# Performance work log

Measured on AMD Instinct MI355X. Metric: run time of the kernel, lower is better.

Reference implementation:

```python
import jax, jax.numpy as jnp
import numpy as np

N = 100000      # number of entities
E = 400000      # number of edges (before self-loops)
D = 200         # feature_dim
D0 = 100        # init_fea_dim
NREL = 475      # 2*num_rels + 1 (self-loop relation = NREL-1)
NBR = 100       # num_base_r
B = 1024        # query batch
L = 2           # number of cells / layers
EPS = 1e-5


def _bn(x, g, b):
    # BatchNorm1d, training-mode batch statistics (biased var), per-feature affine
    m = jnp.mean(x, axis=0)
    v = jnp.var(x, axis=0)
    return (x - m) * jax.lax.rsqrt(v + EPS) * g + b


def setup_inputs() -> dict:
    key = jax.random.key(0)
    ks = jax.random.split(key, 12)
    return {
        # graph (edge list form of the DGL graph g)
        "src_id": jax.random.randint(ks[0], (E,), 0, N),
        "dst_id": jax.random.randint(ks[1], (E,), 0, N),
        "e_type": jax.random.randint(ks[2], (E,), 0, NREL - 1),  # NREL-1 reserved for self-loop
        # link-prediction queries
        "subj": jax.random.randint(ks[3], (B,), 0, N),
        "rel": jax.random.randint(ks[4], (B,), 0, NREL),
        # learned parameters
        "emb_h": jax.random.normal(ks[5], (N, D0), dtype=jnp.float32) * 0.02,
        "emb_e": jax.random.normal(ks[6], (NBR, D), dtype=jnp.float32) * 0.1,
        "lin_w": jax.random.normal(ks[7], (D0, D), dtype=jnp.float32) * (1.0 / np.sqrt(D0)),
        "lin_b": jnp.zeros((D,), dtype=jnp.float32),
        "rel_wt": jax.random.normal(ks[8], (NREL, NBR), dtype=jnp.float32) * 0.1,
        "w_rel": jax.random.normal(ks[9], (D, D), dtype=jnp.float32) * (1.0 / np.sqrt(D)),
        # per-cell params, stacked over L layers
        "agg_bn_g": jnp.ones((L, D), dtype=jnp.float32),
        "agg_bn_b": jnp.zeros((L, D), dtype=jnp.float32),
        "cell_bn_g": jnp.ones((L, D), dtype=jnp.float32),
        "cell_bn_b": jnp.zeros((L, D), dtype=jnp.float32),
        "concat_w": jax.random.normal(ks[10], (L, D, D), dtype=jnp.float32) * (1.0 / np.sqrt(D)),
        "concat_b": jnp.zeros((L, D), dtype=jnp.float32),
    }


def reference(src_id, dst_id, e_type, subj, rel,
              emb_h, emb_e, lin_w, lin_b, rel_wt, w_rel,
              agg_bn_g, agg_bn_b, cell_bn_g, cell_bn_b, concat_w, concat_b):
    nodes = jnp.arange(N, dtype=src_id.dtype)
    # append self-loops for every node, with the dedicated self-loop relation id
    src_f = jnp.concatenate([src_id, nodes])                      # [E+N]
    dst_f = jnp.concatenate([dst_id, nodes])                      # [E+N]
    et_f = jnp.concatenate([e_type, jnp.full((N,), NREL - 1, dtype=e_type.dtype)])

    all_ent = emb_h @ lin_w + lin_b                               # [N, D]
    rel_embed = rel_wt @ emb_e                                    # [NREL, D]

    for i in range(L):
        src_emb = all_ent[src_f]                                  # [E+N, D] per-edge gather
        hr = rel_embed[et_f]                                      # [E+N, D] per-edge gather
        zero_out = src_emb * hr                                   # pre_mult op (no BN/ReLU)
        agg = jax.ops.segment_sum(zero_out, dst_f, num_segments=N)  # edge -> node aggregation
        agg = jax.nn.relu(_bn(agg, agg_bn_g[i], agg_bn_b[i]))     # OpModule BN + ReLU
        h = agg @ concat_w[i] + concat_b[i]                       # Cell concat Linear (1 concat node)
        all_ent = jax.nn.relu(_bn(h, cell_bn_g[i], cell_bn_b[i]))  # Cell BN + ReLU
        rel_embed = rel_embed @ w_rel                             # per-layer relation transform

    # DistMult score function: [B, N]
    score = (all_ent[subj] * rel_embed[rel]) @ all_ent.T
    return score
```

## Files before the change

kernel.cpp:

```cpp
#include <hip/hip_runtime.h>


#define N_ENT  100000
#define N_EDGE 400000
#define N_EF   500000
#define D_     200
#define D0_    100
#define NREL_  475
#define B_     1024
#define GSTAT  1024
#define KP_D   224
#define KP_D0  128

typedef unsigned short ushort_t;
typedef __attribute__((ext_vector_type(8))) short bf16x8;
typedef __attribute__((ext_vector_type(4))) float f32x4;

__device__ __forceinline__ ushort_t f2bf(float x) {
  unsigned u = __float_as_uint(x);
  return (ushort_t)((u + 0x7FFFu + ((u >> 16) & 1u)) >> 16);
}
__device__ __forceinline__ float bf2f(ushort_t h) {
  return __uint_as_float(((unsigned)h) << 16);
}

__device__ __forceinline__ void gld16(const void* g, void* l) {
  __builtin_amdgcn_global_load_lds(
      (const __attribute__((address_space(1))) unsigned*)g,
      (__attribute__((address_space(3))) unsigned*)l, 16, 0, 0);
}


__global__ void k_hist(const int* __restrict__ dst_id, int* __restrict__ cnt) {
  int e = blockIdx.x * 256 + threadIdx.x;
  if (e < N_EF) {
    int d = (e < N_EDGE) ? dst_id[e] : (e - N_EDGE);
    atomicAdd(&cnt[d], 1);
  }
}

__global__ __launch_bounds__(256) void k_scan_block(const int* __restrict__ cnt,
                                                    int* __restrict__ rp,
                                                    int* __restrict__ bsum) {
  __shared__ int sm[256];
  int tid = threadIdx.x;
  int base = blockIdx.x * 1024 + tid * 4;
  int v0 = (base + 0 < N_ENT) ? cnt[base + 0] : 0;
  int v1 = (base + 1 < N_ENT) ? cnt[base + 1] : 0;
  int v2 = (base + 2 < N_ENT) ? cnt[base + 2] : 0;
  int v3 = (base + 3 < N_ENT) ? cnt[base + 3] : 0;
  int tsum = v0 + v1 + v2 + v3;
  sm[tid] = tsum;
  __syncthreads();
  for (int off = 1; off < 256; off <<= 1) {
    int t = (tid >= off) ? sm[tid - off] : 0;
    __syncthreads();
    sm[tid] += t;
    __syncthreads();
  }
  int run = sm[tid] - tsum;
  if (base + 0 < N_ENT) { rp[base + 0] = run; } run += v0;
  if (base + 1 < N_ENT) { rp[base + 1] = run; } run += v1;
  if (base + 2 < N_ENT) { rp[base + 2] = run; } run += v2;
  if (base + 3 < N_ENT) { rp[base + 3] = run; }
  if (tid == 255) bsum[blockIdx.x] = sm[255];
}

__global__ void k_scan_tops(int* __restrict__ bsum, int nb) {
  __shared__ int sm[256];
  int tid = threadIdx.x;
  int v = (tid < nb) ? bsum[tid] : 0;
  sm[tid] = v;
  __syncthreads();
  for (int off = 1; off < 256; off <<= 1) {
    int t = (tid >= off) ? sm[tid - off] : 0;
    __syncthreads();
    sm[tid] += t;
    __syncthreads();
  }
  if (tid < nb) bsum[tid] = sm[tid] - v;
}

__global__ void k_scan_add(int* __restrict__ rp, const int* __restrict__ bsum,
                           int* __restrict__ cursor) {
  int i = blockIdx.x * 256 + threadIdx.x;
  if (i < N_ENT) {
    int r = rp[i] + bsum[i >> 10];
    rp[i] = r;
    cursor[i] = r;
  }
}

__global__ void k_fill(const int* __restrict__ src_id, const int* __restrict__ dst_id,
                       const int* __restrict__ e_type, int* __restrict__ cursor,
                       int* __restrict__ cs, int* __restrict__ ct) {
  int e = blockIdx.x * 256 + threadIdx.x;
  if (e < N_EF) {
    int s, d, t;
    if (e < N_EDGE) { s = src_id[e]; d = dst_id[e]; t = e_type[e]; }
    else            { s = e - N_EDGE; d = s; t = NREL_ - 1; }
    int pos = atomicAdd(&cursor[d], 1);
    cs[pos] = s;
    ct[pos] = t;
  }
}


__global__ __launch_bounds__(256) void k_aggregate(const float* __restrict__ ent,
                                                   const float* __restrict__ relE,
                                                   const int* __restrict__ rp,
                                                   const int* __restrict__ cnt,
                                                   const int* __restrict__ cs,
                                                   const int* __restrict__ ct,
                                                   float* __restrict__ out) {
  int n = blockIdx.x;
  int f = threadIdx.x;
  if (f >= D_) return;
  int s0 = rp[n], e0 = s0 + cnt[n];
  float acc0 = 0.f, acc1 = 0.f;
  int idx = s0;
  for (; idx + 2 <= e0; idx += 2) {
    int sA = cs[idx], tA = ct[idx];
    int sB = cs[idx + 1], tB = ct[idx + 1];
    float eA = ent[(long)sA * D_ + f], rA = relE[(long)tA * D_ + f];
    float eB = ent[(long)sB * D_ + f], rB = relE[(long)tB * D_ + f];
    acc0 = fmaf(eA, rA, acc0);
    acc1 = fmaf(eB, rB, acc1);
  }
  if (idx < e0) {
    int sA = cs[idx], tA = ct[idx];
    acc0 = fmaf(ent[(long)sA * D_ + f], relE[(long)tA * D_ + f], acc0);
  }
  out[(long)n * D_ + f] = acc0 + acc1;
}

__global__ __launch_bounds__(256) void k_colstats(const float* __restrict__ X,
                                                  double* __restrict__ part) {
  int f = threadIdx.x;
  if (f >= D_) return;
  double s = 0.0, s2 = 0.0;
  for (int r = blockIdx.x; r < N_ENT; r += GSTAT) {
    float v = X[(long)r * D_ + f];
    s += v;
    s2 += (double)v * v;
  }
  part[(long)blockIdx.x * (2 * D_) + f] = s;
  part[(long)blockIdx.x * (2 * D_) + D_ + f] = s2;
}

__global__ __launch_bounds__(256) void k_bn_fin(const double* __restrict__ part,
                                                const float* __restrict__ g,
                                                const float* __restrict__ b,
                                                float* __restrict__ scale,
                                                float* __restrict__ shift) {
  int f = blockIdx.x;
  int tid = threadIdx.x;
  double S = 0.0, S2 = 0.0;
  for (int i = tid; i < GSTAT; i += 256) {
    S += part[(long)i * (2 * D_) + f];
    S2 += part[(long)i * (2 * D_) + D_ + f];
  }
  __shared__ double smS[256], smS2[256];
  smS[tid] = S; smS2[tid] = S2;
  __syncthreads();
  for (int off = 128; off > 0; off >>= 1) {
    if (tid < off) { smS[tid] += smS[tid + off]; smS2[tid] += smS2[tid + off]; }
    __syncthreads();
  }
  if (tid == 0) {
    double mean = smS[0] / N_ENT;
    double var = smS2[0] / N_ENT - mean * mean;
    double inv = 1.0 / sqrt(var + 1e-5);
    float sc = g[f] * (float)inv;
    scale[f] = sc;
    shift[f] = b[f] - (float)mean * sc;
  }
}

template <bool SPLIT>
__global__ void k_norm_relu(float* __restrict__ X, const float* __restrict__ scale,
                            const float* __restrict__ shift,
                            ushort_t* __restrict__ H, ushort_t* __restrict__ L) {
  if (!SPLIT) {
    const long total = (long)N_ENT * D_ / 4;
    for (long i4 = (long)blockIdx.x * 256 + threadIdx.x; i4 < total;
         i4 += (long)gridDim.x * 256) {
      float4 v = ((float4*)X)[i4];
      int fb = (int)((i4 * 4) % D_);
      v.x = fmaxf(fmaf(v.x, scale[fb + 0], shift[fb + 0]), 0.f);
      v.y = fmaxf(fmaf(v.y, scale[fb + 1], shift[fb + 1]), 0.f);
      v.z = fmaxf(fmaf(v.z, scale[fb + 2], shift[fb + 2]), 0.f);
      v.w = fmaxf(fmaf(v.w, scale[fb + 3], shift[fb + 3]), 0.f);
      ((float4*)X)[i4] = v;
    }
  } else {
    const long total = (long)N_ENT * (KP_D / 4);
    for (long i4 = (long)blockIdx.x * 256 + threadIdx.x; i4 < total;
         i4 += (long)gridDim.x * 256) {
      int r = (int)(i4 / (KP_D / 4));
      int c4 = (int)(i4 % (KP_D / 4)) * 4;
      float vv[4] = {0.f, 0.f, 0.f, 0.f};
      if (c4 < D_) {
        float4 v = *(float4*)(X + (long)r * D_ + c4);
        vv[0] = fmaxf(fmaf(v.x, scale[c4 + 0], shift[c4 + 0]), 0.f);
        vv[1] = fmaxf(fmaf(v.y, scale[c4 + 1], shift[c4 + 1]), 0.f);
        vv[2] = fmaxf(fmaf(v.z, scale[c4 + 2], shift[c4 + 2]), 0.f);
        vv[3] = fmaxf(fmaf(v.w, scale[c4 + 3], shift[c4 + 3]), 0.f);
        float4 o = make_float4(vv[0], vv[1], vv[2], vv[3]);
        *(float4*)(X + (long)r * D_ + c4) = o;
      }
      unsigned hpack0, hpack1, lpack0, lpack1;
      ushort_t h[4], l[4];
#pragma unroll
      for (int t = 0; t < 4; t++) {
        h[t] = f2bf(vv[t]);
        l[t] = f2bf(vv[t] - bf2f(h[t]));
      }
      hpack0 = (unsigned)h[0] | ((unsigned)h[1] << 16);
      hpack1 = (unsigned)h[2] | ((unsigned)h[3] << 16);
      lpack0 = (unsigned)l[0] | ((unsigned)l[1] << 16);
      lpack1 = (unsigned)l[2] | ((unsigned)l[3] << 16);
      long o = (long)r * KP_D + c4;
      *(uint2*)(H + o) = make_uint2(hpack0, hpack1);
      *(uint2*)(L + o) = make_uint2(lpack0, lpack1);
    }
  }
}


__global__ void k_split(const float* __restrict__ X, int R, int K, int Kp,
                        ushort_t* __restrict__ H, ushort_t* __restrict__ L,
                        const float* __restrict__ scale,
                        const float* __restrict__ shift) {
  int kq = Kp >> 2;
  long i = (long)blockIdx.x * 256 + threadIdx.x;
  if (i >= (long)R * kq) return;
  int r = (int)(i / kq);
  int k4 = (int)(i % kq) * 4;
  float vv[4] = {0.f, 0.f, 0.f, 0.f};
  if (k4 < K) {
    float4 v = *(const float4*)(X + (long)r * K + k4);
    vv[0] = v.x; vv[1] = v.y; vv[2] = v.z; vv[3] = v.w;
    if (scale) {
#pragma unroll
      for (int t = 0; t < 4; t++)
        vv[t] = fmaxf(fmaf(vv[t], scale[k4 + t], shift[k4 + t]), 0.f);
    }
  }
  ushort_t h[4], l[4];
#pragma unroll
  for (int t = 0; t < 4; t++) {
    h[t] = f2bf(vv[t]);
    l[t] = f2bf(vv[t] - bf2f(h[t]));
  }
  long o = (long)r * Kp + k4;
  *(uint2*)(H + o) = make_uint2((unsigned)h[0] | ((unsigned)h[1] << 16),
                                (unsigned)h[2] | ((unsigned)h[3] << 16));
  *(uint2*)(L + o) = make_uint2((unsigned)l[0] | ((unsigned)l[1] << 16),
                                (unsigned)l[2] | ((unsigned)l[3] << 16));
}

__global__ void k_tsplit(const float* __restrict__ W, int K, int Nc, int Kp,
                         ushort_t* __restrict__ H, ushort_t* __restrict__ L) {
  int i = blockIdx.x * 256 + threadIdx.x;
  if (i >= Nc * Kp) return;
  int n = i / Kp, kp = i - n * Kp;
  float v = (kp < K) ? W[(long)kp * Nc + n] : 0.f;
  ushort_t h = f2bf(v);
  H[i] = h;
  L[i] = f2bf(v - bf2f(h));
}

__global__ void k_qsplit(const float* __restrict__ ent, const float* __restrict__ relE,
                         const int* __restrict__ subj, const int* __restrict__ rel,
                         ushort_t* __restrict__ H, ushort_t* __restrict__ L) {
  int i = blockIdx.x * 256 + threadIdx.x;
  if (i >= B_ * KP_D) return;
  int b = i / KP_D, kp = i - b * KP_D;
  float v = 0.f;
  if (kp < D_)
    v = ent[(long)subj[b] * D_ + kp] * relE[(long)rel[b] * D_ + kp];
  ushort_t h = f2bf(v);
  H[i] = h;
  L[i] = f2bf(v - bf2f(h));
}

template <bool HAS_BIAS, bool SWZ>
__global__ __launch_bounds__(256, 2) void k_mfma_abt(
    const ushort_t* __restrict__ Ah, const ushort_t* __restrict__ Al,
    const ushort_t* __restrict__ Bh, const ushort_t* __restrict__ Bl,
    float* __restrict__ C, int M, int Nc, int Kp, long ldc,
    const float* __restrict__ bias) {
  __shared__ ushort_t lds[4 * 128 * 32];
  const int tid = threadIdx.x;
  const int wave = tid >> 6, lane = tid & 63;
  int bxi, byi;
  if (SWZ) {
    int orig = blockIdx.x;
    int cpx = gridDim.x >> 3;
    int swz = (orig & 7) * cpx + (orig >> 3);
    bxi = swz & 7;
    byi = swz >> 3;
  } else {
    bxi = blockIdx.x;
    byi = blockIdx.y;
  }
  const int bm = bxi * 128, bn = byi * 128;
  const int wr = (wave >> 1) * 64, wc = (wave & 1) * 64;
  const int l15 = lane & 15, l4 = lane >> 4;

  f32x4 acc[4][4] = {};

  for (int kc = 0; kc < Kp; kc += 32) {
#pragma unroll
    for (int j = 0; j < 8; ++j) {
      int c = wave * 8 + j;
      int buf = c >> 3;
      int r = (c & 7) * 16 + (lane >> 2);
      int sg = (lane & 3) ^ ((r >> 1) & 3);
      const ushort_t* bp;
      int rowg;
      if (buf == 0)      { bp = Ah; rowg = bm + r; if (rowg > M - 1) rowg = M - 1; }
      else if (buf == 1) { bp = Al; rowg = bm + r; if (rowg > M - 1) rowg = M - 1; }
      else if (buf == 2) { bp = Bh; rowg = bn + r; if (rowg > Nc - 1) rowg = Nc - 1; }
      else               { bp = Bl; rowg = bn + r; if (rowg > Nc - 1) rowg = Nc - 1; }
      const ushort_t* g = bp + (long)rowg * Kp + kc + sg * 8;
      gld16(g, lds + c * 512);
    }
    __syncthreads();

    bf16x8 a_h[4], a_l[4], b_h[4], b_l[4];
#pragma unroll
    for (int i = 0; i < 4; i++) {
      int rA = wr + i * 16 + l15;
      int sA = (l4 ^ ((rA >> 1) & 3)) * 8;
      a_h[i] = *(const bf16x8*)(lds + rA * 32 + sA);
      a_l[i] = *(const bf16x8*)(lds + 4096 + rA * 32 + sA);
      int rB = wc + i * 16 + l15;
      int sB = (l4 ^ ((rB >> 1) & 3)) * 8;
      b_h[i] = *(const bf16x8*)(lds + 8192 + rB * 32 + sB);
      b_l[i] = *(const bf16x8*)(lds + 12288 + rB * 32 + sB);
    }
#pragma unroll
    for (int i = 0; i < 4; i++)
#pragma unroll
      for (int j = 0; j < 4; j++) {
        acc[i][j] = __builtin_amdgcn_mfma_f32_16x16x32_bf16(a_h[i], b_h[j], acc[i][j], 0, 0, 0);
        acc[i][j] = __builtin_amdgcn_mfma_f32_16x16x32_bf16(a_l[i], b_h[j], acc[i][j], 0, 0, 0);
        acc[i][j] = __builtin_amdgcn_mfma_f32_16x16x32_bf16(a_h[i], b_l[j], acc[i][j], 0, 0, 0);
      }
    __syncthreads();
  }

#pragma unroll
  for (int i = 0; i < 4; i++) {
    int mrow = bm + wr + i * 16 + l4 * 4;
#pragma unroll
    for (int j = 0; j < 4; j++) {
      int n = bn + wc + j * 16 + l15;
      if (n >= Nc) continue;
      float bb = HAS_BIAS ? bias[n] : 0.f;
#pragma unroll
      for (int v = 0; v < 4; v++) {
        int m = mrow + v;
        if (m < M) C[(long)m * ldc + n] = acc[i][j][v] + bb;
      }
    }
  }
}

template <int TM, int TN>
__global__ __launch_bounds__(256) void k_gemm_abt(
    const float* __restrict__ A, const float* __restrict__ Bm, float* __restrict__ C,
    int M, int Nc, int K, long ldc) {
  constexpr int BM = TM * 16, BN = TN * 16, KC = 20;
  __shared__ float As[BM * KC];
  __shared__ float Bs[BN * KC];
  const int tid = threadIdx.x;
  const int tx = tid & 15, ty = tid >> 4;
  const int bm = blockIdx.x * BM, bn = blockIdx.y * BN;
  float acc[TM][TN];
#pragma unroll
  for (int i = 0; i < TM; i++)
#pragma unroll
    for (int j = 0; j < TN; j++) acc[i][j] = 0.f;
  for (int kc = 0; kc < K; kc += KC) {
    for (int i4 = tid; i4 < BM * 5; i4 += 256) {
      int r = i4 / 5, kq = (i4 - r * 5) * 4;
      int row = bm + r; if (row > M - 1) row = M - 1;
      *(float4*)(As + r * KC + kq) = *(const float4*)(A + (long)row * K + kc + kq);
    }
    for (int i4 = tid; i4 < BN * 5; i4 += 256) {
      int r = i4 / 5, kq = (i4 - r * 5) * 4;
      int row = bn + r; if (row > Nc - 1) row = Nc - 1;
      *(float4*)(Bs + r * KC + kq) = *(const float4*)(Bm + (long)row * K + kc + kq);
    }
    __syncthreads();
#pragma unroll
    for (int k4 = 0; k4 < KC; k4 += 4) {
      float4 af[TM], bf[TN];
#pragma unroll
      for (int i = 0; i < TM; i++) af[i] = *(const float4*)(As + (i * 16 + ty) * KC + k4);
#pragma unroll
      for (int j = 0; j < TN; j++) bf[j] = *(const float4*)(Bs + (j * 16 + tx) * KC + k4);
#pragma unroll
      for (int i = 0; i < TM; i++)
#pragma unroll
        for (int j = 0; j < TN; j++) {
          acc[i][j] = fmaf(af[i].x, bf[j].x, acc[i][j]);
          acc[i][j] = fmaf(af[i].y, bf[j].y, acc[i][j]);
          acc[i][j] = fmaf(af[i].z, bf[j].z, acc[i][j]);
          acc[i][j] = fmaf(af[i].w, bf[j].w, acc[i][j]);
        }
    }
    __syncthreads();
  }
#pragma unroll
  for (int i = 0; i < TM; i++) {
    int m = bm + i * 16 + ty;
    if (m >= M) continue;
#pragma unroll
    for (int j = 0; j < TN; j++) {
      int n = bn + j * 16 + tx;
      if (n < Nc) C[(long)m * ldc + n] = acc[i][j];
    }
  }
}

__global__ void k_transpose(const float* __restrict__ s, float* __restrict__ d, int R, int C) {
  int i = blockIdx.x * 256 + threadIdx.x;
  if (i < R * C) { int r = i / C, c = i - r * C; d[c * R + r] = s[i]; }
}


extern "C" void kernel_launch(void* const* d_in, const int* in_sizes, int n_in,
                              void* d_out, int out_size, void* d_ws, size_t ws_size,
                              hipStream_t stream) {
  const int* src_id = (const int*)d_in[0];
  const int* dst_id = (const int*)d_in[1];
  const int* e_type = (const int*)d_in[2];
  const int* subj = (const int*)d_in[3];
  const int* rel = (const int*)d_in[4];
  const float* emb_h = (const float*)d_in[5];
  const float* emb_e = (const float*)d_in[6];
  const float* lin_w = (const float*)d_in[7];
  const float* lin_b = (const float*)d_in[8];
  const float* rel_wt = (const float*)d_in[9];
  const float* w_rel = (const float*)d_in[10];
  const float* agg_bn_g = (const float*)d_in[11];
  const float* agg_bn_b = (const float*)d_in[12];
  const float* cell_bn_g = (const float*)d_in[13];
  const float* cell_bn_b = (const float*)d_in[14];
  const float* concat_w = (const float*)d_in[15];
  const float* concat_b = (const float*)d_in[16];
  float* out = (float*)d_out;

  char* w = (char*)d_ws;
  ushort_t* ent_h = (ushort_t*)(w + 0);
  ushort_t* ent_l = (ushort_t*)(w + 44800000);
  ushort_t* q_h   = (ushort_t*)(w + 89600000);
  ushort_t* q_l   = (ushort_t*)(w + 90112000);

  char* ob = (char*)d_out;
  float* ent    = (float*)(ob + 0);
  float* tmp    = (float*)(ob + 80000000);
  ushort_t* tmp_h = (ushort_t*)(ob + 160000000);
  ushort_t* tmp_l = (ushort_t*)(ob + 204800000);
  ushort_t* embh_h = (ushort_t*)(ob + 160000000);
  ushort_t* embh_l = (ushort_t*)(ob + 185600000);
  int* counts  = (int*)(ob + 249600000);
  int* row_ptr = (int*)(ob + 250000000);
  int* cursor  = (int*)(ob + 250400000);
  int* csr_src = (int*)(ob + 250800000);
  int* csr_et  = (int*)(ob + 252800000);
  double* part = (double*)(ob + 254800000);
  float* relA  = (float*)(ob + 258100000);
  float* relB  = (float*)(ob + 258480000);
  float* embeT = (float*)(ob + 258860000);
  float* wrT   = (float*)(ob + 258940000);
  ushort_t* linw_h = (ushort_t*)(ob + 259100000);
  ushort_t* linw_l = (ushort_t*)(ob + 259151200);
  ushort_t* cw0_h  = (ushort_t*)(ob + 259202400);
  ushort_t* cw0_l  = (ushort_t*)(ob + 259292000);
  ushort_t* cw1_h  = (ushort_t*)(ob + 259381600);
  ushort_t* cw1_l  = (ushort_t*)(ob + 259471200);
  float* scaleb = (float*)(ob + 259560800);
  float* shiftb = (float*)(ob + 259561696);
  int* bsum     = (int*)(ob + 259562592);

  hipMemsetAsync(counts, 0, N_ENT * sizeof(int), stream);
  k_hist<<<(N_EF + 255) / 256, 256, 0, stream>>>(dst_id, counts);
  const int NB = (N_ENT + 1023) / 1024;
  k_scan_block<<<NB, 256, 0, stream>>>(counts, row_ptr, bsum);
  k_scan_tops<<<1, 256, 0, stream>>>(bsum, NB);
  k_scan_add<<<(N_ENT + 255) / 256, 256, 0, stream>>>(row_ptr, bsum, cursor);
  k_fill<<<(N_EF + 255) / 256, 256, 0, stream>>>(src_id, dst_id, e_type, cursor,
                                                 csr_src, csr_et);

  k_tsplit<<<(D_ * KP_D0 + 255) / 256, 256, 0, stream>>>(lin_w, D0_, D_, KP_D0,
                                                         linw_h, linw_l);
  k_tsplit<<<(D_ * KP_D + 255) / 256, 256, 0, stream>>>(concat_w, D_, D_, KP_D,
                                                        cw0_h, cw0_l);
  k_tsplit<<<(D_ * KP_D + 255) / 256, 256, 0, stream>>>(concat_w + D_ * D_, D_, D_,
                                                        KP_D, cw1_h, cw1_l);
  k_transpose<<<(D0_ * D_ + 255) / 256, 256, 0, stream>>>(emb_e, embeT, D0_, D_);
  k_transpose<<<(D_ * D_ + 255) / 256, 256, 0, stream>>>(w_rel, wrT, D_, D_);

  const int GM = (N_ENT + 127) / 128;
  {
    long tot = (long)N_ENT * (KP_D0 / 4);
    k_split<<<(int)((tot + 255) / 256), 256, 0, stream>>>(emb_h, N_ENT, D0_, KP_D0,
                                                          embh_h, embh_l, nullptr, nullptr);
    k_mfma_abt<true, false><<<dim3(GM, 2), 256, 0, stream>>>(
        embh_h, embh_l, linw_h, linw_l, ent, N_ENT, D_, KP_D0, (long)D_, lin_b);
  }
  k_gemm_abt<8, 4><<<dim3(4, 4), 256, 0, stream>>>(rel_wt, embeT, relA, NREL_, D_,
                                                   D0_, (long)D_);

  float* relCur = relA;
  float* relNxt = relB;
  for (int i = 0; i < 2; i++) {
    k_aggregate<<<N_ENT, 256, 0, stream>>>(ent, relCur, row_ptr, counts, csr_src,
                                           csr_et, tmp);
    k_colstats<<<GSTAT, 256, 0, stream>>>(tmp, part);
    k_bn_fin<<<D_, 256, 0, stream>>>(part, agg_bn_g + i * D_, agg_bn_b + i * D_,
                                     scaleb, shiftb);
    long tot = (long)N_ENT * (KP_D / 4);
    k_split<<<(int)((tot + 255) / 256), 256, 0, stream>>>(tmp, N_ENT, D_, KP_D,
                                                          tmp_h, tmp_l, scaleb, shiftb);
    k_mfma_abt<true, false><<<dim3(GM, 2), 256, 0, stream>>>(
        tmp_h, tmp_l, (i == 0) ? cw0_h : cw1_h, (i == 0) ? cw0_l : cw1_l, ent,
        N_ENT, D_, KP_D, (long)D_, concat_b + i * D_);
    k_colstats<<<GSTAT, 256, 0, stream>>>(ent, part);
    k_bn_fin<<<D_, 256, 0, stream>>>(part, cell_bn_g + i * D_, cell_bn_b + i * D_,
                                     scaleb, shiftb);
    if (i == 0) {
      k_norm_relu<false><<<2048, 256, 0, stream>>>(ent, scaleb, shiftb, nullptr, nullptr);
    } else {
      k_norm_relu<true><<<2048, 256, 0, stream>>>(ent, scaleb, shiftb, ent_h, ent_l);
    }
    k_gemm_abt<8, 4><<<dim3(4, 4), 256, 0, stream>>>(relCur, wrT, relNxt, NREL_, D_,
                                                     D_, (long)D_);
    float* t = relCur; relCur = relNxt; relNxt = t;
  }

  k_qsplit<<<(B_ * KP_D + 255) / 256, 256, 0, stream>>>(ent, relCur, subj, rel,
                                                        q_h, q_l);

  k_mfma_abt<false, true><<<dim3((B_ / 128) * GM), 256, 0, stream>>>(
      q_h, q_l, ent_h, ent_l, out, B_, N_ENT, KP_D, (long)N_ENT, nullptr);
}
```

Before: 1.123 ms.

## Fuse BN+split into GEMM A-load, double-buffer MFMA, fold layer-0 BN into aggregate

The per-layer GEMMs now read fp32 activations directly, apply the BN scale/shift and ReLU, and split to bf16 hi/lo in registers while staging into LDS. This removes the separate k_split passes and their bf16 buffers. The layer-0 cell BN+ReLU is folded into the layer-1 gather, so the standalone normalize pass is dropped. The MFMA kernels gain LDS double buffering to overlap loads with compute, the aggregate loop is unrolled to 4 edges, and colstats uses float4 rows with more blocks. In exchange, the BN transform is recomputed per gathered edge, and the GEMMs use more LDS and registers.

```diff
diff --git a/kernel.cpp b/kernel.cpp
--- a/kernel.cpp
+++ b/kernel.cpp
@@ -8,7 +8,7 @@
 #define D0_    100
 #define NREL_  475
 #define B_     1024
-#define GSTAT  1024
+#define GSTAT2 2048
 #define KP_D   224
 #define KP_D0  128
 
@@ -106,46 +106,68 @@
 }
 
 
+template <bool BN>
 __global__ __launch_bounds__(256) void k_aggregate(const float* __restrict__ ent,
                                                    const float* __restrict__ relE,
                                                    const int* __restrict__ rp,
                                                    const int* __restrict__ cnt,
                                                    const int* __restrict__ cs,
                                                    const int* __restrict__ ct,
-                                                   float* __restrict__ out) {
+                                                   float* __restrict__ out,
+                                                   const float* __restrict__ scale,
+                                                   const float* __restrict__ shift) {
   int n = blockIdx.x;
   int f = threadIdx.x;
   if (f >= D_) return;
+  float sc = 0.f, sh = 0.f;
+  if (BN) { sc = scale[f]; sh = shift[f]; }
   int s0 = rp[n], e0 = s0 + cnt[n];
-  float acc0 = 0.f, acc1 = 0.f;
+  float a0 = 0.f, a1 = 0.f, a2 = 0.f, a3 = 0.f;
   int idx = s0;
-  for (; idx + 2 <= e0; idx += 2) {
-    int sA = cs[idx], tA = ct[idx];
+  for (; idx + 4 <= e0; idx += 4) {
+    int sA = cs[idx + 0], tA = ct[idx + 0];
     int sB = cs[idx + 1], tB = ct[idx + 1];
+    int sC = cs[idx + 2], tC = ct[idx + 2];
+    int sD = cs[idx + 3], tD = ct[idx + 3];
     float eA = ent[(long)sA * D_ + f], rA = relE[(long)tA * D_ + f];
     float eB = ent[(long)sB * D_ + f], rB = relE[(long)tB * D_ + f];
-    acc0 = fmaf(eA, rA, acc0);
-    acc1 = fmaf(eB, rB, acc1);
-  }
-  if (idx < e0) {
+    float eC = ent[(long)sC * D_ + f], rC = relE[(long)tC * D_ + f];
+    float eD = ent[(long)sD * D_ + f], rD = relE[(long)tD * D_ + f];
+    if (BN) {
+      eA = fmaxf(fmaf(eA, sc, sh), 0.f);
+      eB = fmaxf(fmaf(eB, sc, sh), 0.f);
+      eC = fmaxf(fmaf(eC, sc, sh), 0.f);
+      eD = fmaxf(fmaf(eD, sc, sh), 0.f);
+    }
+    a0 = fmaf(eA, rA, a0);
+    a1 = fmaf(eB, rB, a1);
+    a2 = fmaf(eC, rC, a2);
+    a3 = fmaf(eD, rD, a3);
+  }
+  for (; idx < e0; ++idx) {
     int sA = cs[idx], tA = ct[idx];
-    acc0 = fmaf(ent[(long)sA * D_ + f], relE[(long)tA * D_ + f], acc0);
-  }
-  out[(long)n * D_ + f] = acc0 + acc1;
-}
-
-__global__ __launch_bounds__(256) void k_colstats(const float* __restrict__ X,
-                                                  double* __restrict__ part) {
-  int f = threadIdx.x;
-  if (f >= D_) return;
-  double s = 0.0, s2 = 0.0;
-  for (int r = blockIdx.x; r < N_ENT; r += GSTAT) {
-    float v = X[(long)r * D_ + f];
-    s += v;
-    s2 += (double)v * v;
-  }
-  part[(long)blockIdx.x * (2 * D_) + f] = s;
-  part[(long)blockIdx.x * (2 * D_) + D_ + f] = s2;
+    float eA = ent[(long)sA * D_ + f];
+    if (BN) eA = fmaxf(fmaf(eA, sc, sh), 0.f);
+    a0 = fmaf(eA, relE[(long)tA * D_ + f], a0);
+  }
+  out[(long)n * D_ + f] = (a0 + a1) + (a2 + a3);
+}
+
+__global__ __launch_bounds__(64) void k_colstats(const float* __restrict__ X,
+                                                 double* __restrict__ part) {
+  int t = threadIdx.x;
+  if (t >= 50) return;
+  double s0 = 0, s1 = 0, s2 = 0, s3 = 0, q0 = 0, q1 = 0, q2 = 0, q3 = 0;
+  for (int r = blockIdx.x; r < N_ENT; r += GSTAT2) {
+    float4 v = *(const float4*)(X + (long)r * D_ + t * 4);
+    s0 += v.x; q0 += (double)v.x * v.x;
+    s1 += v.y; q1 += (double)v.y * v.y;
+    s2 += v.z; q2 += (double)v.z * v.z;
+    s3 += v.w; q3 += (double)v.w * v.w;
+  }
+  long o = (long)blockIdx.x * 400 + t * 4;
+  part[o + 0] = s0; part[o + 1] = s1; part[o + 2] = s2; part[o + 3] = s3;
+  part[o + 200] = q0; part[o + 201] = q1; part[o + 202] = q2; part[o + 203] = q3;
 }
 
 __global__ __launch_bounds__(256) void k_bn_fin(const double* __restrict__ part,
@@ -156,9 +178,9 @@
   int f = blockIdx.x;
   int tid = threadIdx.x;
   double S = 0.0, S2 = 0.0;
-  for (int i = tid; i < GSTAT; i += 256) {
-    S += part[(long)i * (2 * D_) + f];
-    S2 += part[(long)i * (2 * D_) + D_ + f];
+  for (int i = tid; i < GSTAT2; i += 256) {
+    S += part[(long)i * 400 + f];
+    S2 += part[(long)i * 400 + 200 + f];
   }
   __shared__ double smS[256], smS2[256];
   smS[tid] = S; smS2[tid] = S2;
@@ -177,87 +199,35 @@
   }
 }
 
-template <bool SPLIT>
-__global__ void k_norm_relu(float* __restrict__ X, const float* __restrict__ scale,
-                            const float* __restrict__ shift,
-                            ushort_t* __restrict__ H, ushort_t* __restrict__ L) {
-  if (!SPLIT) {
-    const long total = (long)N_ENT * D_ / 4;
-    for (long i4 = (long)blockIdx.x * 256 + threadIdx.x; i4 < total;
-         i4 += (long)gridDim.x * 256) {
-      float4 v = ((float4*)X)[i4];
-      int fb = (int)((i4 * 4) % D_);
-      v.x = fmaxf(fmaf(v.x, scale[fb + 0], shift[fb + 0]), 0.f);
-      v.y = fmaxf(fmaf(v.y, scale[fb + 1], shift[fb + 1]), 0.f);
-      v.z = fmaxf(fmaf(v.z, scale[fb + 2], shift[fb + 2]), 0.f);
-      v.w = fmaxf(fmaf(v.w, scale[fb + 3], shift[fb + 3]), 0.f);
-      ((float4*)X)[i4] = v;
-    }
-  } else {
-    const long total = (long)N_ENT * (KP_D / 4);
-    for (long i4 = (long)blockIdx.x * 256 + threadIdx.x; i4 < total;
-         i4 += (long)gridDim.x * 256) {
-      int r = (int)(i4 / (KP_D / 4));
-      int c4 = (int)(i4 % (KP_D / 4)) * 4;
-      float vv[4] = {0.f, 0.f, 0.f, 0.f};
-      if (c4 < D_) {
-        float4 v = *(float4*)(X + (long)r * D_ + c4);
-        vv[0] = fmaxf(fmaf(v.x, scale[c4 + 0], shift[c4 + 0]), 0.f);
-        vv[1] = fmaxf(fmaf(v.y, scale[c4 + 1], shift[c4 + 1]), 0.f);
-        vv[2] = fmaxf(fmaf(v.z, scale[c4 + 2], shift[c4 + 2]), 0.f);
-        vv[3] = fmaxf(fmaf(v.w, scale[c4 + 3], shift[c4 + 3]), 0.f);
-        float4 o = make_float4(vv[0], vv[1], vv[2], vv[3]);
-        *(float4*)(X + (long)r * D_ + c4) = o;
-      }
-      unsigned hpack0, hpack1, lpack0, lpack1;
-      ushort_t h[4], l[4];
-#pragma unroll
-      for (int t = 0; t < 4; t++) {
-        h[t] = f2bf(vv[t]);
-        l[t] = f2bf(vv[t] - bf2f(h[t]));
-      }
-      hpack0 = (unsigned)h[0] | ((unsigned)h[1] << 16);
-      hpack1 = (unsigned)h[2] | ((unsigned)h[3] << 16);
-      lpack0 = (unsigned)l[0] | ((unsigned)l[1] << 16);
-      lpack1 = (unsigned)l[2] | ((unsigned)l[3] << 16);
-      long o = (long)r * KP_D + c4;
-      *(uint2*)(H + o) = make_uint2(hpack0, hpack1);
-      *(uint2*)(L + o) = make_uint2(lpack0, lpack1);
-    }
-  }
-}
-
-
-__global__ void k_split(const float* __restrict__ X, int R, int K, int Kp,
-                        ushort_t* __restrict__ H, ushort_t* __restrict__ L,
-                        const float* __restrict__ scale,
-                        const float* __restrict__ shift) {
-  int kq = Kp >> 2;
-  long i = (long)blockIdx.x * 256 + threadIdx.x;
-  if (i >= (long)R * kq) return;
-  int r = (int)(i / kq);
-  int k4 = (int)(i % kq) * 4;
-  float vv[4] = {0.f, 0.f, 0.f, 0.f};
-  if (k4 < K) {
-    float4 v = *(const float4*)(X + (long)r * K + k4);
-    vv[0] = v.x; vv[1] = v.y; vv[2] = v.z; vv[3] = v.w;
-    if (scale) {
-#pragma unroll
-      for (int t = 0; t < 4; t++)
-        vv[t] = fmaxf(fmaf(vv[t], scale[k4 + t], shift[k4 + t]), 0.f);
-    }
-  }
-  ushort_t h[4], l[4];
-#pragma unroll
-  for (int t = 0; t < 4; t++) {
-    h[t] = f2bf(vv[t]);
-    l[t] = f2bf(vv[t] - bf2f(h[t]));
-  }
-  long o = (long)r * Kp + k4;
-  *(uint2*)(H + o) = make_uint2((unsigned)h[0] | ((unsigned)h[1] << 16),
-                                (unsigned)h[2] | ((unsigned)h[3] << 16));
-  *(uint2*)(L + o) = make_uint2((unsigned)l[0] | ((unsigned)l[1] << 16),
-                                (unsigned)l[2] | ((unsigned)l[3] << 16));
+__global__ void k_norm_split(float* __restrict__ X, const float* __restrict__ scale,
+                             const float* __restrict__ shift,
+                             ushort_t* __restrict__ H, ushort_t* __restrict__ L) {
+  const long total = (long)N_ENT * (KP_D / 4);
+  for (long i4 = (long)blockIdx.x * 256 + threadIdx.x; i4 < total;
+       i4 += (long)gridDim.x * 256) {
+    int r = (int)(i4 / (KP_D / 4));
+    int c4 = (int)(i4 % (KP_D / 4)) * 4;
+    float vv[4] = {0.f, 0.f, 0.f, 0.f};
+    if (c4 < D_) {
+      float4 v = *(float4*)(X + (long)r * D_ + c4);
+      vv[0] = fmaxf(fmaf(v.x, scale[c4 + 0], shift[c4 + 0]), 0.f);
+      vv[1] = fmaxf(fmaf(v.y, scale[c4 + 1], shift[c4 + 1]), 0.f);
+      vv[2] = fmaxf(fmaf(v.z, scale[c4 + 2], shift[c4 + 2]), 0.f);
+      vv[3] = fmaxf(fmaf(v.w, scale[c4 + 3], shift[c4 + 3]), 0.f);
+      *(float4*)(X + (long)r * D_ + c4) = make_float4(vv[0], vv[1], vv[2], vv[3]);
+    }
+    ushort_t h[4], l[4];
+#pragma unroll
+    for (int t = 0; t < 4; t++) {
+      h[t] = f2bf(vv[t]);
+      l[t] = f2bf(vv[t] - bf2f(h[t]));
+    }
+    long o = (long)r * KP_D + c4;
+    *(uint2*)(H + o) = make_uint2((unsigned)h[0] | ((unsigned)h[1] << 16),
+                                  (unsigned)h[2] | ((unsigned)h[3] << 16));
+    *(uint2*)(L + o) = make_uint2((unsigned)l[0] | ((unsigned)l[1] << 16),
+                                  (unsigned)l[2] | ((unsigned)l[3] << 16));
+  }
 }
 
 __global__ void k_tsplit(const float* __restrict__ W, int K, int Nc, int Kp,
@@ -285,13 +255,12 @@
   L[i] = f2bf(v - bf2f(h));
 }
 
-template <bool HAS_BIAS, bool SWZ>
-__global__ __launch_bounds__(256, 2) void k_mfma_abt(
+template <bool SWZ>
+__global__ __launch_bounds__(256, 2) void k_mfma_pre(
     const ushort_t* __restrict__ Ah, const ushort_t* __restrict__ Al,
     const ushort_t* __restrict__ Bh, const ushort_t* __restrict__ Bl,
-    float* __restrict__ C, int M, int Nc, int Kp, long ldc,
-    const float* __restrict__ bias) {
-  __shared__ ushort_t lds[4 * 128 * 32];
+    float* __restrict__ C, int M, int Nc, int Kp, long ldc) {
+  __shared__ __align__(16) ushort_t lds[2 * 16384];
   const int tid = threadIdx.x;
   const int wave = tid >> 6, lane = tid & 63;
   int bxi, byi;
@@ -308,10 +277,11 @@
   const int bm = bxi * 128, bn = byi * 128;
   const int wr = (wave >> 1) * 64, wc = (wave & 1) * 64;
   const int l15 = lane & 15, l4 = lane >> 4;
+  const int NT = Kp >> 5;
 
   f32x4 acc[4][4] = {};
 
-  for (int kc = 0; kc < Kp; kc += 32) {
+  auto stage = [&](int kt, int ph) {
 #pragma unroll
     for (int j = 0; j < 8; ++j) {
       int c = wave * 8 + j;
@@ -324,22 +294,27 @@
       else if (buf == 1) { bp = Al; rowg = bm + r; if (rowg > M - 1) rowg = M - 1; }
       else if (buf == 2) { bp = Bh; rowg = bn + r; if (rowg > Nc - 1) rowg = Nc - 1; }
       else               { bp = Bl; rowg = bn + r; if (rowg > Nc - 1) rowg = Nc - 1; }
-      const ushort_t* g = bp + (long)rowg * Kp + kc + sg * 8;
-      gld16(g, lds + c * 512);
-    }
-    __syncthreads();
-
+      gld16(bp + (long)rowg * Kp + kt * 32 + sg * 8, lds + ph * 16384 + c * 512);
+    }
+  };
+
+  stage(0, 0);
+  __syncthreads();
+  int p = 0;
+  for (int t = 0; t < NT; ++t) {
+    if (t + 1 < NT) stage(t + 1, p ^ 1);
+    const ushort_t* base = lds + p * 16384;
     bf16x8 a_h[4], a_l[4], b_h[4], b_l[4];
 #pragma unroll
     for (int i = 0; i < 4; i++) {
       int rA = wr + i * 16 + l15;
       int sA = (l4 ^ ((rA >> 1) & 3)) * 8;
-      a_h[i] = *(const bf16x8*)(lds + rA * 32 + sA);
-      a_l[i] = *(const bf16x8*)(lds + 4096 + rA * 32 + sA);
+      a_h[i] = *(const bf16x8*)(base + rA * 32 + sA);
+      a_l[i] = *(const bf16x8*)(base + 4096 + rA * 32 + sA);
       int rB = wc + i * 16 + l15;
       int sB = (l4 ^ ((rB >> 1) & 3)) * 8;
-      b_h[i] = *(const bf16x8*)(lds + 8192 + rB * 32 + sB);
-      b_l[i] = *(const bf16x8*)(lds + 12288 + rB * 32 + sB);
+      b_h[i] = *(const bf16x8*)(base + 8192 + rB * 32 + sB);
+      b_l[i] = *(const bf16x8*)(base + 12288 + rB * 32 + sB);
     }
 #pragma unroll
     for (int i = 0; i < 4; i++)
@@ -350,6 +325,158 @@
         acc[i][j] = __builtin_amdgcn_mfma_f32_16x16x32_bf16(a_h[i], b_l[j], acc[i][j], 0, 0, 0);
       }
     __syncthreads();
+    p ^= 1;
+  }
+
+#pragma unroll
+  for (int i = 0; i < 4; i++) {
+    int mrow = bm + wr + i * 16 + l4 * 4;
+#pragma unroll
+    for (int j = 0; j < 4; j++) {
+      int n = bn + wc + j * 16 + l15;
+      if (n >= Nc) continue;
+#pragma unroll
+      for (int v = 0; v < 4; v++) {
+        int m = mrow + v;
+        if (m < M) C[(long)m * ldc + n] = acc[i][j][v];
+      }
+    }
+  }
+}
+
+template <bool BN_A, bool HAS_BIAS>
+__global__ __launch_bounds__(256, 2) void k_mfma_af32(
+    const float* __restrict__ A, int lda, int K,
+    const ushort_t* __restrict__ Bh, const ushort_t* __restrict__ Bl,
+    float* __restrict__ C, int M, int Nc, int Kp, long ldc,
+    const float* __restrict__ scale, const float* __restrict__ shift,
+    const float* __restrict__ bias) {
+  __shared__ __align__(16) ushort_t lds[2 * 16384];
+  __shared__ float sc_lds[KP_D], sh_lds[KP_D];
+  const int tid = threadIdx.x;
+  const int wave = tid >> 6, lane = tid & 63;
+  const int bm = blockIdx.x * 128, bn = blockIdx.y * 128;
+  const int wr = (wave >> 1) * 64, wc = (wave & 1) * 64;
+  const int l15 = lane & 15, l4 = lane >> 4;
+  const int NT = Kp >> 5;
+
+  if (BN_A) {
+    for (int i = tid; i < Kp; i += 256) {
+      sc_lds[i] = (i < K) ? scale[i] : 0.f;
+      sh_lds[i] = (i < K) ? shift[i] : 0.f;
+    }
+    __syncthreads();
+  }
+
+  const int ar = tid >> 1;
+  const int acb = (tid & 1) * 16;
+  int arow = bm + ar; if (arow > M - 1) arow = M - 1;
+  const int aswz = (ar >> 1) & 3;
+  const int s0 = (((acb >> 3) + 0) ^ aswz) * 8;
+  const int s1 = (((acb >> 3) + 1) ^ aswz) * 8;
+
+  auto loadA = [&](int kt, float4* va) {
+    int kc = kt * 32 + acb;
+    const float* ap = A + (long)arow * lda + kc;
+    if (kc + 16 <= K) {
+#pragma unroll
+      for (int q = 0; q < 4; q++) va[q] = *(const float4*)(ap + q * 4);
+    } else {
+#pragma unroll
+      for (int q = 0; q < 4; q++) {
+        float t0 = (kc + q * 4 + 0 < K) ? ap[q * 4 + 0] : 0.f;
+        float t1 = (kc + q * 4 + 1 < K) ? ap[q * 4 + 1] : 0.f;
+        float t2 = (kc + q * 4 + 2 < K) ? ap[q * 4 + 2] : 0.f;
+        float t3 = (kc + q * 4 + 3 < K) ? ap[q * 4 + 3] : 0.f;
+        va[q] = make_float4(t0, t1, t2, t3);
+      }
+    }
+  };
+
+  auto writeA = [&](int kt, int ph, float4* va) {
+    float v[16];
+#pragma unroll
+    for (int q = 0; q < 4; q++) {
+      v[q * 4 + 0] = va[q].x; v[q * 4 + 1] = va[q].y;
+      v[q * 4 + 2] = va[q].z; v[q * 4 + 3] = va[q].w;
+    }
+    if (BN_A) {
+      int kc = kt * 32 + acb;
+#pragma unroll
+      for (int e = 0; e < 16; e++) {
+        int col = kc + e;
+        if (col < K) v[e] = fmaxf(fmaf(v[e], sc_lds[col], sh_lds[col]), 0.f);
+      }
+    }
+    unsigned hh[8], ll[8];
+#pragma unroll
+    for (int e = 0; e < 8; e++) {
+      ushort_t h0 = f2bf(v[2 * e]), h1 = f2bf(v[2 * e + 1]);
+      ushort_t l0 = f2bf(v[2 * e] - bf2f(h0)), l1 = f2bf(v[2 * e + 1] - bf2f(h1));
+      hh[e] = (unsigned)h0 | ((unsigned)h1 << 16);
+      ll[e] = (unsigned)l0 | ((unsigned)l1 << 16);
+    }
+    ushort_t* baseA = lds + ph * 16384 + ar * 32;
+    *(uint4*)(baseA + s0) = make_uint4(hh[0], hh[1], hh[2], hh[3]);
+    *(uint4*)(baseA + s1) = make_uint4(hh[4], hh[5], hh[6], hh[7]);
+    ushort_t* baseL = baseA + 4096;
+    *(uint4*)(baseL + s0) = make_uint4(ll[0], ll[1], ll[2], ll[3]);
+    *(uint4*)(baseL + s1) = make_uint4(ll[4], ll[5], ll[6], ll[7]);
+  };
+
+  auto stageB = [&](int kt, int ph) {
+#pragma unroll
+    for (int j = 0; j < 4; ++j) {
+      int c = 16 + wave * 4 + j;
+      int buf = c >> 3;
+      int r = (c & 7) * 16 + (lane >> 2);
+      int sg = (lane & 3) ^ ((r >> 1) & 3);
+      const ushort_t* bp = (buf == 2) ? Bh : Bl;
+      int rowg = bn + r; if (rowg > Nc - 1) rowg = Nc - 1;
+      gld16(bp + (long)rowg * Kp + kt * 32 + sg * 8, lds + ph * 16384 + c * 512);
+    }
+  };
+
+  f32x4 acc[4][4] = {};
+  {
+    float4 va[4];
+    loadA(0, va);
+    writeA(0, 0, va);
+    stageB(0, 0);
+  }
+  __syncthreads();
+  int p = 0;
+  for (int t = 0; t < NT; ++t) {
+    float4 va[4];
+    const bool pre = (t + 1 < NT);
+    if (pre) {
+      loadA(t + 1, va);
+      stageB(t + 1, p ^ 1);
+    }
+    const ushort_t* base = lds + p * 16384;
+    bf16x8 a_h[4], a_l[4], b_h[4], b_l[4];
+#pragma unroll
+    for (int i = 0; i < 4; i++) {
+      int rA = wr + i * 16 + l15;
+      int sA = (l4 ^ ((rA >> 1) & 3)) * 8;
+      a_h[i] = *(const bf16x8*)(base + rA * 32 + sA);
+      a_l[i] = *(const bf16x8*)(base + 4096 + rA * 32 + sA);
+      int rB = wc + i * 16 + l15;
+      int sB = (l4 ^ ((rB >> 1) & 3)) * 8;
+      b_h[i] = *(const bf16x8*)(base + 8192 + rB * 32 + sB);
+      b_l[i] = *(const bf16x8*)(base + 12288 + rB * 32 + sB);
+    }
+#pragma unroll
+    for (int i = 0; i < 4; i++)
+#pragma unroll
+      for (int j = 0; j < 4; j++) {
+        acc[i][j] = __builtin_amdgcn_mfma_f32_16x16x32_bf16(a_h[i], b_h[j], acc[i][j], 0, 0, 0);
+        acc[i][j] = __builtin_amdgcn_mfma_f32_16x16x32_bf16(a_l[i], b_h[j], acc[i][j], 0, 0, 0);
+        acc[i][j] = __builtin_amdgcn_mfma_f32_16x16x32_bf16(a_h[i], b_l[j], acc[i][j], 0, 0, 0);
+      }
+    if (pre) writeA(t + 1, p ^ 1, va);
+    __syncthreads();
+    p ^= 1;
   }
 
 #pragma unroll
@@ -464,29 +591,25 @@
   char* ob = (char*)d_out;
   float* ent    = (float*)(ob + 0);
   float* tmp    = (float*)(ob + 80000000);
-  ushort_t* tmp_h = (ushort_t*)(ob + 160000000);
-  ushort_t* tmp_l = (ushort_t*)(ob + 204800000);
-  ushort_t* embh_h = (ushort_t*)(ob + 160000000);
-  ushort_t* embh_l = (ushort_t*)(ob + 185600000);
-  int* counts  = (int*)(ob + 249600000);
-  int* row_ptr = (int*)(ob + 250000000);
-  int* cursor  = (int*)(ob + 250400000);
-  int* csr_src = (int*)(ob + 250800000);
-  int* csr_et  = (int*)(ob + 252800000);
-  double* part = (double*)(ob + 254800000);
-  float* relA  = (float*)(ob + 258100000);
-  float* relB  = (float*)(ob + 258480000);
-  float* embeT = (float*)(ob + 258860000);
-  float* wrT   = (float*)(ob + 258940000);
-  ushort_t* linw_h = (ushort_t*)(ob + 259100000);
-  ushort_t* linw_l = (ushort_t*)(ob + 259151200);
-  ushort_t* cw0_h  = (ushort_t*)(ob + 259202400);
-  ushort_t* cw0_l  = (ushort_t*)(ob + 259292000);
-  ushort_t* cw1_h  = (ushort_t*)(ob + 259381600);
-  ushort_t* cw1_l  = (ushort_t*)(ob + 259471200);
-  float* scaleb = (float*)(ob + 259560800);
-  float* shiftb = (float*)(ob + 259561696);
-  int* bsum     = (int*)(ob + 259562592);
+  double* part  = (double*)(ob + 160000000);
+  int* counts   = (int*)(ob + 166600000);
+  int* row_ptr  = (int*)(ob + 167000000);
+  int* cursor   = (int*)(ob + 167400000);
+  int* csr_src  = (int*)(ob + 167800000);
+  int* csr_et   = (int*)(ob + 169800000);
+  float* relA   = (float*)(ob + 171800000);
+  float* relB   = (float*)(ob + 172180000);
+  float* embeT  = (float*)(ob + 172560000);
+  float* wrT    = (float*)(ob + 172640000);
+  ushort_t* linw_h = (ushort_t*)(ob + 172800000);
+  ushort_t* linw_l = (ushort_t*)(ob + 172851200);
+  ushort_t* cw0_h  = (ushort_t*)(ob + 172902400);
+  ushort_t* cw0_l  = (ushort_t*)(ob + 172992000);
+  ushort_t* cw1_h  = (ushort_t*)(ob + 173081600);
+  ushort_t* cw1_l  = (ushort_t*)(ob + 173171200);
+  float* scaleb = (float*)(ob + 173260800);
+  float* shiftb = (float*)(ob + 173261824);
+  int* bsum     = (int*)(ob + 173262848);
 
   hipMemsetAsync(counts, 0, N_ENT * sizeof(int), stream);
   k_hist<<<(N_EF + 255) / 256, 256, 0, stream>>>(dst_id, counts);
@@ -507,46 +630,41 @@
   k_transpose<<<(D_ * D_ + 255) / 256, 256, 0, stream>>>(w_rel, wrT, D_, D_);
 
   const int GM = (N_ENT + 127) / 128;
-  {
-    long tot = (long)N_ENT * (KP_D0 / 4);
-    k_split<<<(int)((tot + 255) / 256), 256, 0, stream>>>(emb_h, N_ENT, D0_, KP_D0,
-                                                          embh_h, embh_l, nullptr, nullptr);
-    k_mfma_abt<true, false><<<dim3(GM, 2), 256, 0, stream>>>(
-        embh_h, embh_l, linw_h, linw_l, ent, N_ENT, D_, KP_D0, (long)D_, lin_b);
-  }
+
+  k_mfma_af32<false, true><<<dim3(GM, 2), 256, 0, stream>>>(
+      emb_h, D0_, D0_, linw_h, linw_l, ent, N_ENT, D_, KP_D0, (long)D_,
+      nullptr, nullptr, lin_b);
   k_gemm_abt<8, 4><<<dim3(4, 4), 256, 0, stream>>>(rel_wt, embeT, relA, NREL_, D_,
                                                    D0_, (long)D_);
 
-  float* relCur = relA;
-  float* relNxt = relB;
-  for (int i = 0; i < 2; i++) {
-    k_aggregate<<<N_ENT, 256, 0, stream>>>(ent, relCur, row_ptr, counts, csr_src,
-                                           csr_et, tmp);
-    k_colstats<<<GSTAT, 256, 0, stream>>>(tmp, part);
-    k_bn_fin<<<D_, 256, 0, stream>>>(part, agg_bn_g + i * D_, agg_bn_b + i * D_,
-                                     scaleb, shiftb);
-    long tot = (long)N_ENT * (KP_D / 4);
-    k_split<<<(int)((tot + 255) / 256), 256, 0, stream>>>(tmp, N_ENT, D_, KP_D,
-                                                          tmp_h, tmp_l, scaleb, shiftb);
-    k_mfma_abt<true, false><<<dim3(GM, 2), 256, 0, stream>>>(
-        tmp_h, tmp_l, (i == 0) ? cw0_h : cw1_h, (i == 0) ? cw0_l : cw1_l, ent,
-        N_ENT, D_, KP_D, (long)D_, concat_b + i * D_);
-    k_colstats<<<GSTAT, 256, 0, stream>>>(ent, part);
-    k_bn_fin<<<D_, 256, 0, stream>>>(part, cell_bn_g + i * D_, cell_bn_b + i * D_,
-                                     scaleb, shiftb);
-    if (i == 0) {
-      k_norm_relu<false><<<2048, 256, 0, stream>>>(ent, scaleb, shiftb, nullptr, nullptr);
-    } else {
-      k_norm_relu<true><<<2048, 256, 0, stream>>>(ent, scaleb, shiftb, ent_h, ent_l);
-    }
-    k_gemm_abt<8, 4><<<dim3(4, 4), 256, 0, stream>>>(relCur, wrT, relNxt, NREL_, D_,
-                                                     D_, (long)D_);
-    float* t = relCur; relCur = relNxt; relNxt = t;
-  }
-
-  k_qsplit<<<(B_ * KP_D + 255) / 256, 256, 0, stream>>>(ent, relCur, subj, rel,
+  k_aggregate<false><<<N_ENT, 256, 0, stream>>>(ent, relA, row_ptr, counts,
+                                                csr_src, csr_et, tmp, nullptr, nullptr);
+  k_colstats<<<GSTAT2, 64, 0, stream>>>(tmp, part);
+  k_bn_fin<<<D_, 256, 0, stream>>>(part, agg_bn_g, agg_bn_b, scaleb, shiftb);
+  k_mfma_af32<true, true><<<dim3(GM, 2), 256, 0, stream>>>(
+      tmp, D_, D_, cw0_h, cw0_l, ent, N_ENT, D_, KP_D, (long)D_,
+      scaleb, shiftb, concat_b);
+  k_colstats<<<GSTAT2, 64, 0, stream>>>(ent, part);
+  k_bn_fin<<<D_, 256, 0, stream>>>(part, cell_bn_g, cell_bn_b, scaleb, shiftb);
+  k_gemm_abt<8, 4><<<dim3(4, 4), 256, 0, stream>>>(relA, wrT, relB, NREL_, D_, D_,
+                                                   (long)D_);
+
+  k_aggregate<true><<<N_ENT, 256, 0, stream>>>(ent, relB, row_ptr, counts,
+                                               csr_src, csr_et, tmp, scaleb, shiftb);
+  k_colstats<<<GSTAT2, 64, 0, stream>>>(tmp, part);
+  k_bn_fin<<<D_, 256, 0, stream>>>(part, agg_bn_g + D_, agg_bn_b + D_, scaleb, shiftb);
+  k_mfma_af32<true, true><<<dim3(GM, 2), 256, 0, stream>>>(
+      tmp, D_, D_, cw1_h, cw1_l, ent, N_ENT, D_, KP_D, (long)D_,
+      scaleb, shiftb, concat_b + D_);
+  k_colstats<<<GSTAT2, 64, 0, stream>>>(ent, part);
+  k_bn_fin<<<D_, 256, 0, stream>>>(part, cell_bn_g + D_, cell_bn_b + D_, scaleb, shiftb);
+  k_norm_split<<<2048, 256, 0, stream>>>(ent, scaleb, shiftb, ent_h, ent_l);
+  k_gemm_abt<8, 4><<<dim3(4, 4), 256, 0, stream>>>(relB, wrT, relA, NREL_, D_, D_,
+                                                   (long)D_);
+
+  k_qsplit<<<(B_ * KP_D + 255) / 256, 256, 0, stream>>>(ent, relA, subj, rel,
                                                         q_h, q_l);
 
-  k_mfma_abt<false, true><<<dim3((B_ / 128) * GM), 256, 0, stream>>>(
-      q_h, q_l, ent_h, ent_l, out, B_, N_ENT, KP_D, (long)N_ENT, nullptr);
-}
+  k_mfma_pre<true><<<dim3((B_ / 128) * GM), 256, 0, stream>>>(
+      q_h, q_l, ent_h, ent_l, out, B_, N_ENT, KP_D, (long)N_ENT);
+}
```

After: 1.129 ms. Within noise of the previous version (+0.5%).
